# Kernel optimization log

Measured on AMD Instinct MI355X. Metric: run time of the kernel, lower is better.

The kernel has to match this reference:

```python
import jax, jax.numpy as jnp
import numpy as np

B, L, F, H, VOCAB = 32, 700, 4, 600, 2000  # batch, n_records(max_len), feats/record, hidden, vocab


def setup_inputs() -> dict:
    key = jax.random.key(0)
    ks = jax.random.split(key, 16)
    s = 0.02
    inp = {
        'records': jax.random.randint(ks[0], (B, L, F), 0, VOCAB, dtype=jnp.int64 if jax.config.jax_enable_x64 else jnp.int32),
        'index': jax.random.randint(ks[1], (B,), 0, L, dtype=jnp.int32),
        'emb': jax.random.normal(ks[2], (VOCAB, H), jnp.float32) * s,
        'W_relu': jax.random.normal(ks[3], (4 * H, H), jnp.float32) * s,
        'b_relu': jnp.zeros((H,), jnp.float32),
        'W_lin': jax.random.normal(ks[4], (H, H), jnp.float32) * s,
        'b_lin': jnp.zeros((H,), jnp.float32),
        'W_sig': jax.random.normal(ks[5], (2 * H, H), jnp.float32) * s,
        'b_sig': jnp.zeros((H,), jnp.float32),
        'W_ih': jax.random.normal(ks[6], (H, 4 * H), jnp.float32) * s,
        'W_hh': jax.random.normal(ks[7], (H, 4 * H), jnp.float32) * s,
        'b_ih': jnp.zeros((4 * H,), jnp.float32),
        'b_hh': jnp.zeros((4 * H,), jnp.float32),
        'W_log': jax.random.normal(ks[8], (H, L), jnp.float32) * s,
        'b_log': jnp.zeros((L,), jnp.float32),
    }
    return inp


def _select_content(records, emb, W_relu, b_relu, W_lin, b_lin, W_sig, b_sig):
    # embedding + concat of the 4 record features -> [B, L, 4H]
    embedded = emb[records]                               # [B, L, 4, H]
    emb_cat = embedded.reshape(records.shape[0], records.shape[1], -1)
    emb_relu = jax.nn.relu(emb_cat @ W_relu + b_relu)      # [B, L, H]
    emb_lin = emb_relu @ W_lin + b_lin                     # [B, L, H]
    pre_attn = jnp.einsum('bld,bmd->blm', emb_lin, emb_relu)  # [B, L, L]
    pad = (records.max(axis=2) == 0)                       # [B, L]
    mask = jnp.eye(records.shape[1], dtype=bool)[None] | pad[:, :, None] | pad[:, None, :]
    pre_attn = jnp.where(mask, -jnp.inf, pre_attn)
    attention = jax.nn.softmax(pre_attn, axis=2)
    emb_att = jnp.einsum('blm,bmd->bld', attention, emb_relu)  # [B, L, H]
    gate = jax.nn.sigmoid(jnp.concatenate([emb_relu, emb_att], axis=2) @ W_sig + b_sig)
    return gate * emb_relu                                 # selected_content [B, L, H]


def reference(records, index, emb, W_relu, b_relu, W_lin, b_lin, W_sig, b_sig,
              W_ih, W_hh, b_ih, b_hh, W_log, b_log):
    sc = _select_content(records, emb, W_relu, b_relu, W_lin, b_lin, W_sig, b_sig)
    # init_hidden
    hidden = jnp.mean(sc, axis=1)                          # [B, H]
    cell = jnp.zeros_like(hidden)
    pad_mask = (records.max(axis=2) == 0)                  # [B, L]
    # forward (one pointer step)
    b_idx = jnp.arange(records.shape[0])
    mask = pad_mask.at[b_idx, index].set(True)             # scatter_(1, index, 1)
    x = sc[b_idx, index]                                   # gather -> [B, H]
    gates = x @ W_ih + hidden @ W_hh + b_ih + b_hh         # [B, 4H]
    i, f, g, o = jnp.split(gates, 4, axis=1)               # torch LSTM gate order
    cell = jax.nn.sigmoid(f) * cell + jax.nn.sigmoid(i) * jnp.tanh(g)
    hidden = jax.nn.sigmoid(o) * jnp.tanh(cell)
    logits = hidden @ W_log + b_log                        # [B, max_len]
    masked = jnp.where(mask, -jnp.inf, logits)
    attention = jax.nn.log_softmax(masked, axis=1)         # [B, max_len]
    return attention, hidden, cell
```

## Files before the change

### kernel.cpp

```cpp
#include <hip/hip_runtime.h>
#include <math.h>

typedef unsigned short u16;
typedef _Float16 half8 __attribute__((ext_vector_type(8)));
typedef float f32x4 __attribute__((ext_vector_type(4)));

#define BB 32
#define LL 700
#define HH 600
#define VV 2000
#define H4 2400

#define O_SCAT   0L
#define O_LINH   57344000L
#define O_R1     86016000L
#define O_ATTNH  112896000L
#define O_ERT    144435200L
#define O_EMBH   171468800L
#define O_W2T    174028800L
#define O_WLT    177100800L
#define O_WST    177920000L
#define O_BL     179456000L
#define O_PAD    179458560L
#define O_GATES  179624960L
#define O_WIHT   179932160L
#define O_WLOGT  186076160L
#define O_XCAT   186977280L
#define O_HID16  187059200L
#define O_GLOG   187100160L
#define O_XMEAN  187190272L

__device__ inline u16 f2h(float x) { _Float16 h = (_Float16)x; u16 u; __builtin_memcpy(&u, &h, 2); return u; }
__device__ inline float h2f(u16 u) { _Float16 h; __builtin_memcpy(&h, &u, 2); return (float)h; }

__device__ __forceinline__ void gll16(const u16* g, u16* l) {
    __builtin_amdgcn_global_load_lds(
        (__attribute__((address_space(1))) void*)g,
        (__attribute__((address_space(3))) void*)l, 16, 0, 0);
}

template<int EPI>
__global__ __launch_bounds__(512, 4) void hgemm_v2(
    const u16* __restrict__ A, const u16* __restrict__ B,
    u16* __restrict__ C16, const float* __restrict__ bias,
    const u16* __restrict__ gate, int ldg,
    float* __restrict__ xmean,
    int M, int N, int Kp, int lda, int ldb, int ldc,
    long sAz, long sBz, long sCz)
{
    const int bz = blockIdx.z;
    A += sAz * bz;  B += sBz * bz;  C16 += sCz * bz;

    __shared__ __align__(16) u16 As[16384];
    __shared__ __align__(16) u16 Bs[16384];

    const int tid = threadIdx.x;

    const int nx = gridDim.x, ny = gridDim.y;
    const int bid = blockIdx.y * nx + blockIdx.x;
    const int fg  = ny >> 3;
    const int gsz = nx << 3;
    int m_i, n_i;
    if (bid < fg * gsz) {
        int g = bid / gsz, r = bid - g * gsz;
        m_i = (g << 3) + (r & 7);
        n_i = r >> 3;
    } else {
        m_i = bid / nx;
        n_i = bid - m_i * nx;
    }
    const int m0 = m_i << 7, n0 = n_i << 7;

    const int wave = tid >> 6, lane = tid & 63;
    const int fr = lane & 15, q = lane >> 4;
    const int s0 = (q ^ (fr & 7)) << 3;
    const int wm = (wave >> 2) << 6;
    const int wn = (wave & 3) << 5;

    const int srow = lane >> 3;
    const int kx   = ((lane & 7) ^ srow) << 3;
    int ra0 = m0 + (wave << 4) + srow;       if (ra0 > M - 1) ra0 = M - 1;
    int ra1 = m0 + (wave << 4) + 8 + srow;   if (ra1 > M - 1) ra1 = M - 1;
    int rb0 = n0 + (wave << 4) + srow;       if (rb0 > N - 1) rb0 = N - 1;
    int rb1 = n0 + (wave << 4) + 8 + srow;   if (rb1 > N - 1) rb1 = N - 1;
    const u16* gA0 = A + (long)ra0 * lda + kx;
    const u16* gA1 = A + (long)ra1 * lda + kx;
    const u16* gB0 = B + (long)rb0 * ldb + kx;
    const u16* gB1 = B + (long)rb1 * ldb + kx;
    u16* sAw = (u16*)As + (wave << 10);
    u16* sBw = (u16*)Bs + (wave << 10);

    f32x4 acc[4][2];
    #pragma unroll
    for (int i = 0; i < 4; ++i)
        #pragma unroll
        for (int j = 0; j < 2; ++j) acc[i][j] = (f32x4)0.f;

    const int nk = Kp >> 6;

    gll16(gA0, sAw);  gll16(gA1, sAw + 512);
    gll16(gB0, sBw);  gll16(gB1, sBw + 512);
    __syncthreads();

    for (int t = 0; t < nk; ++t) {
        const int cur = (t & 1) << 13;
        if (t + 1 < nk) {
            const int nxt = cur ^ 8192;
            const long ko = (long)(t + 1) << 6;
            gll16(gA0 + ko, sAw + nxt);  gll16(gA1 + ko, sAw + nxt + 512);
            gll16(gB0 + ko, sBw + nxt);  gll16(gB1 + ko, sBw + nxt + 512);
        }
        #pragma unroll
        for (int half = 0; half < 2; ++half) {
            const int sh = s0 ^ (half << 5);
            half8 af[4], bf[2];
            #pragma unroll
            for (int i = 0; i < 4; ++i)
                af[i] = *(const half8*)&As[cur + ((wm + (i << 4) + fr) << 6) + sh];
            #pragma unroll
            for (int j = 0; j < 2; ++j)
                bf[j] = *(const half8*)&Bs[cur + ((wn + (j << 4) + fr) << 6) + sh];
            #pragma unroll
            for (int i = 0; i < 4; ++i)
                #pragma unroll
                for (int j = 0; j < 2; ++j)
                    acc[i][j] = __builtin_amdgcn_mfma_f32_16x16x32_f16(af[i], bf[j], acc[i][j], 0, 0, 0);
        }
        __syncthreads();
    }

    const int lr = (lane >> 4) << 2;

    int  bb0 = 0, bound = 0;
    bool interior = false;
    if (EPI == 2) {
        const int mlo = m0 + wm, mhi = m0 + wm + 63;
        bb0   = mlo / 700;
        bound = (bb0 + 1) * 700;
        interior = (mhi < bound) && (mhi < M);
    }

    #pragma unroll
    for (int j = 0; j < 2; ++j) {
        int n = n0 + wn + (j << 4) + fr;
        if (n >= N) continue;
        float bv = bias ? bias[n] : 0.f;

        if (EPI == 2 && interior) {
            float ps = 0.f;
            #pragma unroll
            for (int i = 0; i < 4; ++i) {
                #pragma unroll
                for (int r = 0; r < 4; ++r) {
                    int m = m0 + wm + (i << 4) + lr + r;
                    float v = acc[i][j][r] + bv;
                    float sg = 1.f / (1.f + expf(-v));
                    float scv = sg * h2f(gate[(long)m * ldg + n]);
                    C16[(long)m * ldc + n] = f2h(scv);
                    ps += scv;
                }
            }
            ps += __shfl_xor(ps, 16);
            ps += __shfl_xor(ps, 32);
            if (q == 0) atomicAdd(&xmean[bb0 * 640 + n], ps);
        } else {
            float ps = 0.f;
            int   cb = -1;
            #pragma unroll
            for (int i = 0; i < 4; ++i) {
                #pragma unroll
                for (int r = 0; r < 4; ++r) {
                    int m = m0 + wm + (i << 4) + lr + r;
                    if (m >= M) continue;
                    long off = (long)m * ldc + n;
                    float v = acc[i][j][r] + bv;
                    if (EPI == 1) C16[off] = f2h(v);
                    if (EPI == 2) {
                        float sg = 1.f / (1.f + expf(-v));
                        float scv = sg * h2f(gate[(long)m * ldg + n]);
                        C16[off] = f2h(scv);
                        int b = (m < bound) ? bb0 : bb0 + 1;
                        if (b != cb) {
                            if (cb >= 0) atomicAdd(&xmean[cb * 640 + n], ps);
                            cb = b;  ps = 0.f;
                        }
                        ps += scv;
                    }
                }
            }
            if (EPI == 2 && cb >= 0) atomicAdd(&xmean[cb * 640 + n], ps);
        }
    }
}

__global__ __launch_bounds__(256) void sgemm_k(
    const u16* __restrict__ A, const u16* __restrict__ B, float* __restrict__ C,
    int N, int Kseg, int lda, int ldb, int ldc)
{
    const int wave = threadIdx.x >> 6, lane = threadIdx.x & 63;
    const int fr = lane & 15, q8 = (lane >> 4) << 3;
    int n = blockIdx.x * 64 + wave * 16 + fr;
    int nc = (n < N) ? n : N - 1;
    const int k0 = blockIdx.y * Kseg;
    const u16* pa0 = A + (long)fr * lda + q8;
    const u16* pa1 = A + (long)(fr + 16) * lda + q8;
    const u16* pb  = B + (long)nc * ldb + q8;
    f32x4 acc0 = (f32x4)0.f, acc1 = (f32x4)0.f;
    #pragma unroll 2
    for (int k = k0; k < k0 + Kseg; k += 32) {
        half8 a0 = *(const half8*)(pa0 + k);
        half8 a1 = *(const half8*)(pa1 + k);
        half8 bv = *(const half8*)(pb + k);
        acc0 = __builtin_amdgcn_mfma_f32_16x16x32_f16(a0, bv, acc0, 0, 0, 0);
        acc1 = __builtin_amdgcn_mfma_f32_16x16x32_f16(a1, bv, acc1, 0, 0, 0);
    }
    if (n >= N) return;
    const int mr = (lane >> 4) << 2;
    #pragma unroll
    for (int r = 0; r < 4; ++r) {
        atomicAdd(&C[(long)(mr + r) * ldc + n], acc0[r]);
        atomicAdd(&C[(long)(mr + r + 16) * ldc + n], acc1[r]);
    }
}

__global__ __launch_bounds__(256) void prep_k(
    const float* __restrict__ emb, const float* __restrict__ W_relu,
    const float* __restrict__ W_lin, const float* __restrict__ W_sig,
    const float* __restrict__ W_ih, const float* __restrict__ W_hh,
    const float* __restrict__ W_log, const float* __restrict__ b_lin,
    const float* __restrict__ b_ih, const float* __restrict__ b_hh,
    const float* __restrict__ b_log,
    u16* __restrict__ embh, u16* __restrict__ w2t, u16* __restrict__ wlt,
    u16* __restrict__ wst, u16* __restrict__ wiht, u16* __restrict__ wlogt,
    float* __restrict__ bl640, float* __restrict__ gates, float* __restrict__ glog,
    float* __restrict__ xmean)
{
    __shared__ float t[32][33];
    const int z = blockIdx.z, bx = blockIdx.x, by = blockIdx.y;
    const int tid = threadIdx.x;

    if (z == 10) {
        int r = by * 32 + (tid >> 5), c = bx * 32 + (tid & 31);
        #pragma unroll
        for (int dy = 0; dy < 32; dy += 8) {
            int rr = r + dy;
            if (rr < VV && c < 640)
                embh[(long)rr * 640 + c] = (c < 600) ? f2h(emb[(long)rr * 600 + c]) : 0;
        }
        return;
    }
    if (z == 11) {
        long idx = ((long)bx * 75 + by) * 256 + tid;
        const long NG = 640 + (long)BB * H4;
        const long NL = NG + (long)BB * 704;
        const long NX = NL + (long)BB * 640;
        if (idx < 640) {
            bl640[idx] = (idx < 600) ? b_lin[idx] : 0.f;
        } else if (idx < NG) {
            long i = idx - 640;
            int n = (int)(i % H4);
            gates[i] = b_ih[n] + b_hh[n];
        } else if (idx < NL) {
            long i = idx - NG;
            int l = (int)(i % 704);
            glog[i] = (l < 700) ? b_log[l] : 0.f;
        } else if (idx < NX) {
            xmean[idx - NL] = 0.f;
        }
        return;
    }

    const float* s; u16* d;
    int R, C, lds_, ldo, Rpad, Cpad;
    if (z < 4)      { s = W_relu + 360000L * z; d = w2t + 384000L * z;
                      R = 600; C = 600; lds_ = 600; ldo = 640;  Rpad = 640; Cpad = 600; }
    else if (z == 4){ s = W_lin;           d = wlt;
                      R = 600; C = 600; lds_ = 600; ldo = 640;  Rpad = 640; Cpad = 640; }
    else if (z == 5){ s = W_sig;           d = wst;
                      R = 600; C = 600; lds_ = 600; ldo = 1280; Rpad = 640; Cpad = 600; }
    else if (z == 6){ s = W_sig + 360000;  d = wst + 640;
                      R = 600; C = 600; lds_ = 600; ldo = 1280; Rpad = 640; Cpad = 600; }
    else if (z == 7){ s = W_ih;            d = wiht;
                      R = 600; C = H4;  lds_ = H4;  ldo = 1280; Rpad = 640; Cpad = H4; }
    else if (z == 8){ s = W_hh;            d = wiht + 640;
                      R = 600; C = H4;  lds_ = H4;  ldo = 1280; Rpad = 640; Cpad = H4; }
    else            { s = W_log;           d = wlogt;
                      R = 600; C = 700; lds_ = 700; ldo = 640;  Rpad = 640; Cpad = 704; }

    int r0 = bx * 32, c0 = by * 32;
    if (r0 >= Rpad || c0 >= Cpad) return;
    int tx = tid & 31, ty = tid >> 5;
    #pragma unroll
    for (int dy = 0; dy < 32; dy += 8) {
        int r = r0 + ty + dy, c = c0 + tx;
        t[ty + dy][tx] = (r < R && c < C) ? s[(long)r * lds_ + c] : 0.f;
    }
    __syncthreads();
    #pragma unroll
    for (int dy = 0; dy < 32; dy += 8) {
        int c = c0 + ty + dy, r = r0 + tx;
        if (r < Rpad && c < Cpad) d[(long)c * ldo + r] = f2h(t[tx][ty + dy]);
    }
}

__global__ __launch_bounds__(320) void gather_relu_k(
    const int* __restrict__ rec, const u16* __restrict__ Ph,
    const float* __restrict__ b_relu, u16* __restrict__ scat, float* __restrict__ pad)
{
    int row = blockIdx.x;
    int t = threadIdx.x;
    int r0 = rec[row * 4 + 0], r1 = rec[row * 4 + 1];
    int r2 = rec[row * 4 + 2], r3 = rec[row * 4 + 3];
    u16* srow = scat + (long)row * 1280;
    if (t < 300) {
        int h = t << 1;
        uint a0 = *(const uint*)&Ph[(long)r0 * H4 + h];
        uint a1 = *(const uint*)&Ph[(long)r1 * H4 + 600 + h];
        uint a2 = *(const uint*)&Ph[(long)r2 * H4 + 1200 + h];
        uint a3 = *(const uint*)&Ph[(long)r3 * H4 + 1800 + h];
        float lo = b_relu[h]     + h2f((u16)a0) + h2f((u16)a1) + h2f((u16)a2) + h2f((u16)a3);
        float hi = b_relu[h + 1] + h2f((u16)(a0 >> 16)) + h2f((u16)(a1 >> 16))
                                 + h2f((u16)(a2 >> 16)) + h2f((u16)(a3 >> 16));
        uint o = (uint)f2h(fmaxf(lo, 0.f)) | ((uint)f2h(fmaxf(hi, 0.f)) << 16);
        *(uint*)&srow[h] = o;
    } else {
        int i = t - 300;
        *(uint*)&srow[600 + (i << 1)]  = 0;
        *(uint*)&srow[1240 + (i << 1)] = 0;
    }
    if (t == 0) {
        int mx = max(max(r0, r1), max(r2, r3));
        pad[row] = (mx == 0) ? 1.f : 0.f;
    }
}

__global__ __launch_bounds__(256) void post4_k(
    u16* __restrict__ attnh, const float* __restrict__ pad,
    const u16* __restrict__ scat, u16* __restrict__ erT)
{
    __shared__ float smem[1056];
    const int bidf = blockIdx.x;
    const int tid  = threadIdx.x;

    if (bidf < 5600) {
        const int bx = bidf % 175, b = bidf / 175;
        const float* pb = pad + b * LL;
        for (int e = tid; e < 704; e += 256)
            smem[e] = (e < LL) ? pb[e] : 1.f;
        __syncthreads();

        const int wave = tid >> 6, lane = tid & 63;
        const int l = bx * 4 + wave;
        u16* row = attnh + (long)b * (LL * 704) + (long)l * 704;
        const bool rowpad = smem[l] != 0.f;

        float v[12];
        float mx = -INFINITY;
        #pragma unroll
        for (int i = 0; i < 6; ++i) {
            int e0 = (lane + (i << 6)) << 1;
            float x0 = -INFINITY, x1 = -INFINITY;
            if (e0 < 704) {
                uint u = *(const uint*)&row[e0];
                if (!(rowpad || e0 == l || smem[e0] != 0.f)) x0 = h2f((u16)u);
                int e1 = e0 + 1;
                if (!(rowpad || e1 == l || smem[e1] != 0.f)) x1 = h2f((u16)(u >> 16));
            }
            v[2 * i] = x0;  v[2 * i + 1] = x1;
            mx = fmaxf(mx, fmaxf(x0, x1));
        }
        #pragma unroll
        for (int m = 32; m > 0; m >>= 1) mx = fmaxf(mx, __shfl_xor(mx, m));
        mx = fmaxf(mx, -1e30f);

        float sum = 0.f;
        #pragma unroll
        for (int i = 0; i < 12; ++i) { v[i] = expf(v[i] - mx); sum += v[i]; }
        #pragma unroll
        for (int m = 32; m > 0; m >>= 1) sum += __shfl_xor(sum, m);
        float inv = (sum > 0.f) ? 1.f / sum : 0.f;

        #pragma unroll
        for (int i = 0; i < 6; ++i) {
            int e0 = (lane + (i << 6)) << 1;
            if (e0 < 704) {
                uint u = (uint)f2h(v[2 * i] * inv) | ((uint)f2h(v[2 * i + 1] * inv) << 16);
                *(uint*)&row[e0] = u;
            }
        }
    } else {
        int tt = bidf - 5600;
        const int bx = tt % 22;  tt /= 22;
        const int by = tt % 19;
        const int bz = tt / 19;
        float (*tr)[33] = (float(*)[33])smem;
        const u16* s = scat + (long)LL * 1280 * bz;
        u16* d = erT + (long)HH * 704 * bz;
        int r0 = bx * 32, c0 = by * 32;
        int tx = tid & 31, ty = tid >> 5;
        #pragma unroll
        for (int dy = 0; dy < 32; dy += 8) {
            int r = r0 + ty + dy, c = c0 + tx;
            tr[ty + dy][tx] = (r < LL && c < HH) ? h2f(s[(long)r * 1280 + c]) : 0.f;
        }
        __syncthreads();
        #pragma unroll
        for (int dy = 0; dy < 32; dy += 8) {
            int c = c0 + ty + dy, r = r0 + tx;
            if (r < 704 && c < HH) d[(long)c * 704 + r] = f2h(tr[tx][ty + dy]);
        }
    }
}

__global__ __launch_bounds__(256) void xcat_k(const u16* __restrict__ sc,
                                              const int* __restrict__ index,
                                              const float* __restrict__ xmean,
                                              u16* __restrict__ xcat)
{
    int b = blockIdx.y;
    if (blockIdx.x == 3) {
        const u16* src = sc + ((long)b * LL + index[b]) * HH;
        u16* dst = xcat + b * 1280;
        for (int j = threadIdx.x; j < 1280; j += 256) {
            if (j < 600) dst[j] = src[j];
            else if (j < 640) dst[j] = 0;
            else if (j >= 1240) dst[j] = 0;
        }
        return;
    }
    int h = blockIdx.x * 256 + threadIdx.x;
    if (h >= HH) return;
    xcat[b * 1280 + 640 + h] = f2h(xmean[b * 640 + h] * (1.f / 700.f));
}

__global__ void lstm_act_k(const float* __restrict__ gates,
                           float* __restrict__ out_hid, float* __restrict__ out_cell,
                           u16* __restrict__ hid16)
{
    int h = blockIdx.x * 256 + threadIdx.x;
    int b = blockIdx.y;
    if (h >= 640) return;
    if (h >= HH) { hid16[b * 640 + h] = 0; return; }
    const float* g = gates + b * H4;
    float gi = g[h], gg = g[1200 + h], go = g[1800 + h];
    float c = (1.f / (1.f + expf(-gi))) * tanhf(gg);
    float hd = (1.f / (1.f + expf(-go))) * tanhf(c);
    out_hid[b * HH + h] = hd;
    out_cell[b * HH + h] = c;
    hid16[b * 640 + h] = f2h(hd);
}

__global__ __launch_bounds__(256) void logsoftmax_k(const float* __restrict__ glog,
                                                    const float* __restrict__ pad,
                                                    const int* __restrict__ index,
                                                    float* __restrict__ out)
{
    int b = blockIdx.x;
    int t = threadIdx.x;
    int idx = index[b];
    __shared__ float red[256];
    float v[3];
    float mx = -INFINITY;
    #pragma unroll
    for (int ii = 0; ii < 3; ++ii) {
        int l = ii * 256 + t;
        float x = -INFINITY;
        if (l < LL && !(pad[b * LL + l] != 0.f || l == idx)) x = glog[b * 704 + l];
        v[ii] = x;
        mx = fmaxf(mx, x);
    }
    red[t] = mx; __syncthreads();
    for (int s = 128; s > 0; s >>= 1) {
        if (t < s) red[t] = fmaxf(red[t], red[t + s]);
        __syncthreads();
    }
    mx = red[0]; __syncthreads();
    float sum = 0.f;
    #pragma unroll
    for (int ii = 0; ii < 3; ++ii) {
        int l = ii * 256 + t;
        if (l < LL) sum += expf(v[ii] - mx);
    }
    red[t] = sum; __syncthreads();
    for (int s = 128; s > 0; s >>= 1) {
        if (t < s) red[t] += red[t + s];
        __syncthreads();
    }
    float lse = mx + logf(red[0]);
    #pragma unroll
    for (int ii = 0; ii < 3; ++ii) {
        int l = ii * 256 + t;
        if (l < LL) out[b * LL + l] = fmaxf(v[ii] - lse, -1e30f);
    }
}

extern "C" void kernel_launch(void* const* d_in, const int* in_sizes, int n_in,
                              void* d_out, int out_size, void* d_ws, size_t ws_size,
                              hipStream_t stream)
{
    const int*   records = (const int*)d_in[0];
    const int*   index   = (const int*)d_in[1];
    const float* emb     = (const float*)d_in[2];
    const float* W_relu  = (const float*)d_in[3];
    const float* b_relu  = (const float*)d_in[4];
    const float* W_lin   = (const float*)d_in[5];
    const float* b_lin   = (const float*)d_in[6];
    const float* W_sig   = (const float*)d_in[7];
    const float* b_sig   = (const float*)d_in[8];
    const float* W_ih    = (const float*)d_in[9];
    const float* W_hh    = (const float*)d_in[10];
    const float* b_ih    = (const float*)d_in[11];
    const float* b_hh    = (const float*)d_in[12];
    const float* W_log   = (const float*)d_in[13];
    const float* b_log   = (const float*)d_in[14];

    char* ws = (char*)d_ws;
    u16*   scat   = (u16*)(ws + O_SCAT);
    u16*   linh   = (u16*)(ws + O_LINH);
    u16*   Ph     = (u16*)(ws + O_R1);
    u16*   sc16   = (u16*)(ws + O_R1);
    u16*   attnh  = (u16*)(ws + O_ATTNH);
    u16*   erT    = (u16*)(ws + O_ERT);
    u16*   embh   = (u16*)(ws + O_EMBH);
    u16*   w2t    = (u16*)(ws + O_W2T);
    u16*   wlt    = (u16*)(ws + O_WLT);
    u16*   wst    = (u16*)(ws + O_WST);
    float* bl640  = (float*)(ws + O_BL);
    float* pad    = (float*)(ws + O_PAD);
    float* gates  = (float*)(ws + O_GATES);
    u16*   wiht   = (u16*)(ws + O_WIHT);
    u16*   wlogt  = (u16*)(ws + O_WLOGT);
    u16*   xcat   = (u16*)(ws + O_XCAT);
    u16*   hid16  = (u16*)(ws + O_HID16);
    float* glog   = (float*)(ws + O_GLOG);
    float* xmean  = (float*)(ws + O_XMEAN);

    float* out      = (float*)d_out;
    float* out_attn = out;
    float* out_hid  = out + BB * LL;
    float* out_cell = out + BB * LL + BB * HH;

    prep_k<<<dim3(20, 75, 12), 256, 0, stream>>>(
        emb, W_relu, W_lin, W_sig, W_ih, W_hh, W_log, b_lin, b_ih, b_hh, b_log,
        embh, w2t, wlt, wst, wiht, wlogt, bl640, gates, glog, xmean);

    hgemm_v2<1><<<dim3(19, 16, 1), 512, 0, stream>>>(
        embh, w2t, Ph, nullptr, nullptr, 0, nullptr,
        VV, H4, 640, 640, 640, H4, 0L, 0L, 0L);

    gather_relu_k<<<dim3(BB * LL), 320, 0, stream>>>(records, Ph, b_relu, scat, pad);

    hgemm_v2<1><<<dim3(5, 175, 1), 512, 0, stream>>>(
        scat, wlt, linh, bl640, nullptr, 0, nullptr,
        BB * LL, 640, 640, 1280, 640, 640, 0L, 0L, 0L);

    hgemm_v2<1><<<dim3(6, 6, BB), 512, 0, stream>>>(
        linh, scat, attnh, nullptr, nullptr, 0, nullptr,
        LL, LL, 640, 640, 1280, 704, (long)LL * 640, (long)LL * 1280, (long)LL * 704);

    post4_k<<<dim3(5600 + 22 * 19 * BB), 256, 0, stream>>>(attnh, pad, scat, erT);

    hgemm_v2<1><<<dim3(5, 6, BB), 512, 0, stream>>>(
        attnh, erT, scat + 640, nullptr, nullptr, 0, nullptr,
        LL, HH, 704, 704, 704, 1280, (long)LL * 704, (long)HH * 704, (long)LL * 1280);

    hgemm_v2<2><<<dim3(5, 175, 1), 512, 0, stream>>>(
        scat, wst, sc16, b_sig, scat, 1280, xmean,
        BB * LL, HH, 1280, 1280, 1280, 600, 0L, 0L, 0L);

    xcat_k<<<dim3(4, BB), 256, 0, stream>>>(sc16, index, xmean, xcat);
    sgemm_k<<<dim3(38, 5), 256, 0, stream>>>(
        xcat, wiht, gates, H4, 256, 1280, 1280, H4);
    lstm_act_k<<<dim3(3, BB), 256, 0, stream>>>(gates, out_hid, out_cell, hid16);
    sgemm_k<<<dim3(11, 5), 256, 0, stream>>>(
        hid16, wlogt, glog, LL, 128, 640, 640, 704);
    logsoftmax_k<<<dim3(BB), 256, 0, stream>>>(glog, pad, index, out_attn);
}
```

Baseline: 407.7 us.

## Fuse erT transpose into lin GEMM launch and merge tail kernels cooperatively

The scat-to-erT transpose moves out of the post-softmax kernel and into extra blocks of the linear-projection GEMM launch. Those blocks run alongside the GEMM tiles, and the softmax becomes its own kernel. The five small tail kernels (xcat, two skinny GEMMs, LSTM activation, log-softmax) are merged into one cooperative kernel that separates phases with grid.sync, cutting launch overhead. The cost is grid-sync latency, plus transpose blocks that must request the GEMM's large LDS and 512-thread footprint, which may reduce their occupancy.

```diff
diff --git a/kernel.cpp b/kernel.cpp
--- a/kernel.cpp
+++ b/kernel.cpp
@@ -1,5 +1,8 @@
 #include <hip/hip_runtime.h>
+#include <hip/hip_cooperative_groups.h>
 #include <math.h>
+
+namespace cg = cooperative_groups;
 
 typedef unsigned short u16;
 typedef _Float16 half8 __attribute__((ext_vector_type(8)));
@@ -39,25 +42,51 @@
         (__attribute__((address_space(3))) void*)l, 16, 0, 0);
 }
 
-template<int EPI>
+template<int EPI, int FUSET>
 __global__ __launch_bounds__(512, 4) void hgemm_v2(
     const u16* __restrict__ A, const u16* __restrict__ B,
     u16* __restrict__ C16, const float* __restrict__ bias,
     const u16* __restrict__ gate, int ldg,
     float* __restrict__ xmean,
     int M, int N, int Kp, int lda, int ldb, int ldc,
-    long sAz, long sBz, long sCz)
-{
+    long sAz, long sBz, long sCz,
+    const u16* __restrict__ tsrc, u16* __restrict__ tdst, int gemm_blocks)
+{
+    __shared__ __align__(16) u16 As[16384];
+    __shared__ __align__(16) u16 Bs[16384];
+
+    if (FUSET && (int)blockIdx.x >= gemm_blocks) {
+        float (*trf)[33] = (float(*)[33])As;
+        int tt = blockIdx.x - gemm_blocks;
+        const int bx = tt % 22;  tt /= 22;
+        const int by = tt % 19;
+        const int bz2 = tt / 19;
+        const u16* s = tsrc + (long)LL * 1280 * bz2;
+        u16* d = tdst + (long)HH * 704 * bz2;
+        const int r0 = bx << 5, c0 = by << 5;
+        const int tx = threadIdx.x & 31, ty = threadIdx.x >> 5;
+        #pragma unroll
+        for (int dy = 0; dy < 32; dy += 16) {
+            int r = r0 + ty + dy, c = c0 + tx;
+            trf[ty + dy][tx] = (r < LL && c < HH) ? h2f(s[(long)r * 1280 + c]) : 0.f;
+        }
+        __syncthreads();
+        #pragma unroll
+        for (int dy = 0; dy < 32; dy += 16) {
+            int c = c0 + ty + dy, r = r0 + tx;
+            if (r < 704 && c < HH) d[(long)c * 704 + r] = f2h(trf[tx][ty + dy]);
+        }
+        return;
+    }
+
     const int bz = blockIdx.z;
     A += sAz * bz;  B += sBz * bz;  C16 += sCz * bz;
 
-    __shared__ __align__(16) u16 As[16384];
-    __shared__ __align__(16) u16 Bs[16384];
-
     const int tid = threadIdx.x;
 
-    const int nx = gridDim.x, ny = gridDim.y;
-    const int bid = blockIdx.y * nx + blockIdx.x;
+    const int nx = FUSET ? 5 : gridDim.x;
+    const int ny = FUSET ? 175 : gridDim.y;
+    const int bid = FUSET ? (int)blockIdx.x : (int)(blockIdx.y * nx + blockIdx.x);
     const int fg  = ny >> 3;
     const int gsz = nx << 3;
     int m_i, n_i;
@@ -193,15 +222,15 @@
     }
 }
 
-__global__ __launch_bounds__(256) void sgemm_k(
-    const u16* __restrict__ A, const u16* __restrict__ B, float* __restrict__ C,
-    int N, int Kseg, int lda, int ldb, int ldc)
-{
-    const int wave = threadIdx.x >> 6, lane = threadIdx.x & 63;
+__device__ __forceinline__ void sgemm_body(
+    int bx, int by, const u16* A, const u16* B, float* C,
+    int N, int Kseg, int lda, int ldb, int ldc, int tid)
+{
+    const int wave = tid >> 6, lane = tid & 63;
     const int fr = lane & 15, q8 = (lane >> 4) << 3;
-    int n = blockIdx.x * 64 + wave * 16 + fr;
+    int n = bx * 64 + wave * 16 + fr;
     int nc = (n < N) ? n : N - 1;
-    const int k0 = blockIdx.y * Kseg;
+    const int k0 = by * Kseg;
     const u16* pa0 = A + (long)fr * lda + q8;
     const u16* pa1 = A + (long)(fr + 16) * lda + q8;
     const u16* pb  = B + (long)nc * ldb + q8;
@@ -220,6 +249,101 @@
     for (int r = 0; r < 4; ++r) {
         atomicAdd(&C[(long)(mr + r) * ldc + n], acc0[r]);
         atomicAdd(&C[(long)(mr + r + 16) * ldc + n], acc1[r]);
+    }
+}
+
+__global__ __launch_bounds__(256) void tail_k(
+    const u16* __restrict__ sc16, const int* __restrict__ index,
+    const float* __restrict__ xmean, u16* __restrict__ xcat,
+    const u16* __restrict__ wiht, float* __restrict__ gates,
+    float* __restrict__ out_hid, float* __restrict__ out_cell,
+    u16* __restrict__ hid16, const u16* __restrict__ wlogt,
+    float* __restrict__ glog, const float* __restrict__ pad,
+    float* __restrict__ out_attn)
+{
+    cg::grid_group grid = cg::this_grid();
+    const int fb  = blockIdx.x;
+    const int tid = threadIdx.x;
+
+    if (fb < 128) {
+        int bxx = fb & 3, b = fb >> 2;
+        if (bxx == 3) {
+            const u16* src = sc16 + ((long)b * LL + index[b]) * HH;
+            u16* dst = xcat + b * 1280;
+            for (int j = tid; j < 1280; j += 256) {
+                if (j < 600) dst[j] = src[j];
+                else if (j < 640) dst[j] = 0;
+                else if (j >= 1240) dst[j] = 0;
+            }
+        } else {
+            int h = bxx * 256 + tid;
+            if (h < HH) xcat[b * 1280 + 640 + h] = f2h(xmean[b * 640 + h] * (1.f / 700.f));
+        }
+    }
+    grid.sync();
+
+    if (fb < 190) sgemm_body(fb % 38, fb / 38, xcat, wiht, gates, H4, 256, 1280, 1280, H4, tid);
+    grid.sync();
+
+    if (fb < 96) {
+        int b = fb / 3;
+        int h = (fb % 3) * 256 + tid;
+        if (h < 640) {
+            if (h >= HH) {
+                hid16[b * 640 + h] = 0;
+            } else {
+                const float* g = gates + b * H4;
+                float gi = g[h], gg = g[1200 + h], go = g[1800 + h];
+                float c = (1.f / (1.f + expf(-gi))) * tanhf(gg);
+                float hd = (1.f / (1.f + expf(-go))) * tanhf(c);
+                out_hid[b * HH + h] = hd;
+                out_cell[b * HH + h] = c;
+                hid16[b * 640 + h] = f2h(hd);
+            }
+        }
+    }
+    grid.sync();
+
+    if (fb < 55) sgemm_body(fb % 11, fb / 11, hid16, wlogt, glog, LL, 128, 640, 640, 704, tid);
+    grid.sync();
+
+    if (fb < 32) {
+        int b = fb;
+        int idx = index[b];
+        __shared__ float red[256];
+        float v[3];
+        float mx = -INFINITY;
+        #pragma unroll
+        for (int ii = 0; ii < 3; ++ii) {
+            int l = ii * 256 + tid;
+            float x = -INFINITY;
+            if (l < LL && !(pad[b * LL + l] != 0.f || l == idx)) x = glog[b * 704 + l];
+            v[ii] = x;
+            mx = fmaxf(mx, x);
+        }
+        red[tid] = mx; __syncthreads();
+        for (int s = 128; s > 0; s >>= 1) {
+            if (tid < s) red[tid] = fmaxf(red[tid], red[tid + s]);
+            __syncthreads();
+        }
+        mx = red[0]; __syncthreads();
+        float sum = 0.f;
+        #pragma unroll
+        for (int ii = 0; ii < 3; ++ii) {
+            int l = ii * 256 + tid;
+            if (l < LL) sum += expf(v[ii] - mx);
+        }
+        red[tid] = sum; __syncthreads();
+        for (int s = 128; s > 0; s >>= 1) {
+            if (tid < s) red[tid] += red[tid + s];
+            __syncthreads();
+        }
+        float lse = mx + logf(red[0]);
+        #pragma unroll
+        for (int ii = 0; ii < 3; ++ii) {
+            int l = ii * 256 + tid;
+            if (l < LL) out_attn[b * LL + l] = fmaxf(v[ii] - lse, -1e30f);
+        }
     }
 }
 
@@ -334,163 +458,55 @@
     }
 }
 
-__global__ __launch_bounds__(256) void post4_k(
-    u16* __restrict__ attnh, const float* __restrict__ pad,
-    const u16* __restrict__ scat, u16* __restrict__ erT)
-{
-    __shared__ float smem[1056];
-    const int bidf = blockIdx.x;
-    const int tid  = threadIdx.x;
-
-    if (bidf < 5600) {
-        const int bx = bidf % 175, b = bidf / 175;
-        const float* pb = pad + b * LL;
-        for (int e = tid; e < 704; e += 256)
-            smem[e] = (e < LL) ? pb[e] : 1.f;
-        __syncthreads();
-
-        const int wave = tid >> 6, lane = tid & 63;
-        const int l = bx * 4 + wave;
-        u16* row = attnh + (long)b * (LL * 704) + (long)l * 704;
-        const bool rowpad = smem[l] != 0.f;
-
-        float v[12];
-        float mx = -INFINITY;
-        #pragma unroll
-        for (int i = 0; i < 6; ++i) {
-            int e0 = (lane + (i << 6)) << 1;
-            float x0 = -INFINITY, x1 = -INFINITY;
-            if (e0 < 704) {
-                uint u = *(const uint*)&row[e0];
-                if (!(rowpad || e0 == l || smem[e0] != 0.f)) x0 = h2f((u16)u);
-                int e1 = e0 + 1;
-                if (!(rowpad || e1 == l || smem[e1] != 0.f)) x1 = h2f((u16)(u >> 16));
-            }
-            v[2 * i] = x0;  v[2 * i + 1] = x1;
-            mx = fmaxf(mx, fmaxf(x0, x1));
-        }
-        #pragma unroll
-        for (int m = 32; m > 0; m >>= 1) mx = fmaxf(mx, __shfl_xor(mx, m));
-        mx = fmaxf(mx, -1e30f);
-
-        float sum = 0.f;
-        #pragma unroll
-        for (int i = 0; i < 12; ++i) { v[i] = expf(v[i] - mx); sum += v[i]; }
-        #pragma unroll
-        for (int m = 32; m > 0; m >>= 1) sum += __shfl_xor(sum, m);
-        float inv = (sum > 0.f) ? 1.f / sum : 0.f;
-
-        #pragma unroll
-        for (int i = 0; i < 6; ++i) {
-            int e0 = (lane + (i << 6)) << 1;
-            if (e0 < 704) {
-                uint u = (uint)f2h(v[2 * i] * inv) | ((uint)f2h(v[2 * i + 1] * inv) << 16);
-                *(uint*)&row[e0] = u;
-            }
-        }
-    } else {
-        int tt = bidf - 5600;
-        const int bx = tt % 22;  tt /= 22;
-        const int by = tt % 19;
-        const int bz = tt / 19;
-        float (*tr)[33] = (float(*)[33])smem;
-        const u16* s = scat + (long)LL * 1280 * bz;
-        u16* d = erT + (long)HH * 704 * bz;
-        int r0 = bx * 32, c0 = by * 32;
-        int tx = tid & 31, ty = tid >> 5;
-        #pragma unroll
-        for (int dy = 0; dy < 32; dy += 8) {
-            int r = r0 + ty + dy, c = c0 + tx;
-            tr[ty + dy][tx] = (r < LL && c < HH) ? h2f(s[(long)r * 1280 + c]) : 0.f;
-        }
-        __syncthreads();
-        #pragma unroll
-        for (int dy = 0; dy < 32; dy += 8) {
-            int c = c0 + ty + dy, r = r0 + tx;
-            if (r < 704 && c < HH) d[(long)c * 704 + r] = f2h(tr[tx][ty + dy]);
-        }
-    }
-}
-
-__global__ __launch_bounds__(256) void xcat_k(const u16* __restrict__ sc,
-                                              const int* __restrict__ index,
-                                              const float* __restrict__ xmean,
-                                              u16* __restrict__ xcat)
-{
-    int b = blockIdx.y;
-    if (blockIdx.x == 3) {
-        const u16* src = sc + ((long)b * LL + index[b]) * HH;
-        u16* dst = xcat + b * 1280;
-        for (int j = threadIdx.x; j < 1280; j += 256) {
-            if (j < 600) dst[j] = src[j];
-            else if (j < 640) dst[j] = 0;
-            else if (j >= 1240) dst[j] = 0;
-        }
-        return;
-    }
-    int h = blockIdx.x * 256 + threadIdx.x;
-    if (h >= HH) return;
-    xcat[b * 1280 + 640 + h] = f2h(xmean[b * 640 + h] * (1.f / 700.f));
-}
-
-__global__ void lstm_act_k(const float* __restrict__ gates,
-                           float* __restrict__ out_hid, float* __restrict__ out_cell,
-                           u16* __restrict__ hid16)
-{
-    int h = blockIdx.x * 256 + threadIdx.x;
-    int b = blockIdx.y;
-    if (h >= 640) return;
-    if (h >= HH) { hid16[b * 640 + h] = 0; return; }
-    const float* g = gates + b * H4;
-    float gi = g[h], gg = g[1200 + h], go = g[1800 + h];
-    float c = (1.f / (1.f + expf(-gi))) * tanhf(gg);
-    float hd = (1.f / (1.f + expf(-go))) * tanhf(c);
-    out_hid[b * HH + h] = hd;
-    out_cell[b * HH + h] = c;
-    hid16[b * 640 + h] = f2h(hd);
-}
-
-__global__ __launch_bounds__(256) void logsoftmax_k(const float* __restrict__ glog,
-                                                    const float* __restrict__ pad,
-                                                    const int* __restrict__ index,
-                                                    float* __restrict__ out)
-{
-    int b = blockIdx.x;
-    int t = threadIdx.x;
-    int idx = index[b];
-    __shared__ float red[256];
-    float v[3];
+__global__ __launch_bounds__(256) void softmax_w(u16* __restrict__ attnh,
+                                                 const float* __restrict__ pad)
+{
+    __shared__ float smem[704];
+    const int bx = blockIdx.x, b = blockIdx.y;
+    const int tid = threadIdx.x;
+    const float* pb = pad + b * LL;
+    for (int e = tid; e < 704; e += 256)
+        smem[e] = (e < LL) ? pb[e] : 1.f;
+    __syncthreads();
+
+    const int wave = tid >> 6, lane = tid & 63;
+    const int l = bx * 4 + wave;
+    u16* row = attnh + (long)b * (LL * 704) + (long)l * 704;
+    const bool rowpad = smem[l] != 0.f;
+
+    float v[12];
     float mx = -INFINITY;
     #pragma unroll
-    for (int ii = 0; ii < 3; ++ii) {
-        int l = ii * 256 + t;
-        float x = -INFINITY;
-        if (l < LL && !(pad[b * LL + l] != 0.f || l == idx)) x = glog[b * 704 + l];
-        v[ii] = x;
-        mx = fmaxf(mx, x);
-    }
-    red[t] = mx; __syncthreads();
-    for (int s = 128; s > 0; s >>= 1) {
-        if (t < s) red[t] = fmaxf(red[t], red[t + s]);
-        __syncthreads();
-    }
-    mx = red[0]; __syncthreads();
+    for (int i = 0; i < 6; ++i) {
+        int e0 = (lane + (i << 6)) << 1;
+        float x0 = -INFINITY, x1 = -INFINITY;
+        if (e0 < 704) {
+            uint u = *(const uint*)&row[e0];
+            if (!(rowpad || e0 == l || smem[e0] != 0.f)) x0 = h2f((u16)u);
+            int e1 = e0 + 1;
+            if (!(rowpad || e1 == l || smem[e1] != 0.f)) x1 = h2f((u16)(u >> 16));
+        }
+        v[2 * i] = x0;  v[2 * i + 1] = x1;
+        mx = fmaxf(mx, fmaxf(x0, x1));
+    }
+    #pragma unroll
+    for (int m = 32; m > 0; m >>= 1) mx = fmaxf(mx, __shfl_xor(mx, m));
+    mx = fmaxf(mx, -1e30f);
+
     float sum = 0.f;
     #pragma unroll
-    for (int ii = 0; ii < 3; ++ii) {
-        int l = ii * 256 + t;
-        if (l < LL) sum += expf(v[ii] - mx);
-    }
-    red[t] = sum; __syncthreads();
-    for (int s = 128; s > 0; s >>= 1) {
-        if (t < s) red[t] += red[t + s];
-        __syncthreads();
-    }
-    float lse = mx + logf(red[0]);
-    #pragma unroll
-    for (int ii = 0; ii < 3; ++ii) {
-        int l = ii * 256 + t;
-        if (l < LL) out[b * LL + l] = fmaxf(v[ii] - lse, -1e30f);
+    for (int i = 0; i < 12; ++i) { v[i] = expf(v[i] - mx); sum += v[i]; }
+    #pragma unroll
+    for (int m = 32; m > 0; m >>= 1) sum += __shfl_xor(sum, m);
+    float inv = (sum > 0.f) ? 1.f / sum : 0.f;
+
+    #pragma unroll
+    for (int i = 0; i < 6; ++i) {
+        int e0 = (lane + (i << 6)) << 1;
+        if (e0 < 704) {
+            uint u = (uint)f2h(v[2 * i] * inv) | ((uint)f2h(v[2 * i + 1] * inv) << 16);
+            *(uint*)&row[e0] = u;
+        }
     }
 }
 
@@ -544,35 +560,37 @@
         emb, W_relu, W_lin, W_sig, W_ih, W_hh, W_log, b_lin, b_ih, b_hh, b_log,
         embh, w2t, wlt, wst, wiht, wlogt, bl640, gates, glog, xmean);
 
-    hgemm_v2<1><<<dim3(19, 16, 1), 512, 0, stream>>>(
+    hgemm_v2<1, 0><<<dim3(19, 16, 1), 512, 0, stream>>>(
         embh, w2t, Ph, nullptr, nullptr, 0, nullptr,
-        VV, H4, 640, 640, 640, H4, 0L, 0L, 0L);
+        VV, H4, 640, 640, 640, H4, 0L, 0L, 0L, nullptr, nullptr, 0);
 
     gather_relu_k<<<dim3(BB * LL), 320, 0, stream>>>(records, Ph, b_relu, scat, pad);
 
-    hgemm_v2<1><<<dim3(5, 175, 1), 512, 0, stream>>>(
+    hgemm_v2<1, 1><<<dim3(875 + 22 * 19 * BB), 512, 0, stream>>>(
         scat, wlt, linh, bl640, nullptr, 0, nullptr,
-        BB * LL, 640, 640, 1280, 640, 640, 0L, 0L, 0L);
-
-    hgemm_v2<1><<<dim3(6, 6, BB), 512, 0, stream>>>(
+        BB * LL, 640, 640, 1280, 640, 640, 0L, 0L, 0L,
+        scat, erT, 875);
+
+    hgemm_v2<1, 0><<<dim3(6, 6, BB), 512, 0, stream>>>(
         linh, scat, attnh, nullptr, nullptr, 0, nullptr,
-        LL, LL, 640, 640, 1280, 704, (long)LL * 640, (long)LL * 1280, (long)LL * 704);
-
-    post4_k<<<dim3(5600 + 22 * 19 * BB), 256, 0, stream>>>(attnh, pad, scat, erT);
-
-    hgemm_v2<1><<<dim3(5, 6, BB), 512, 0, stream>>>(
+        LL, LL, 640, 640, 1280, 704, (long)LL * 640, (long)LL * 1280, (long)LL * 704,
+        nullptr, nullptr, 0);
+
+    softmax_w<<<dim3(175, BB), 256, 0, stream>>>(attnh, pad);
+
+    hgemm_v2<1, 0><<<dim3(5, 6, BB), 512, 0, stream>>>(
         attnh, erT, scat + 640, nullptr, nullptr, 0, nullptr,
-        LL, HH, 704, 704, 704, 1280, (long)LL * 704, (long)HH * 704, (long)LL * 1280);
-
-    hgemm_v2<2><<<dim3(5, 175, 1), 512, 0, stream>>>(
+        LL, HH, 704, 704, 704, 1280, (long)LL * 704, (long)HH * 704, (long)LL * 1280,
+        nullptr, nullptr, 0);
+
+    hgemm_v2<2, 0><<<dim3(5, 175, 1), 512, 0, stream>>>(
         scat, wst, sc16, b_sig, scat, 1280, xmean,
-        BB * LL, HH, 1280, 1280, 1280, 600, 0L, 0L, 0L);
-
-    xcat_k<<<dim3(4, BB), 256, 0, stream>>>(sc16, index, xmean, xcat);
-    sgemm_k<<<dim3(38, 5), 256, 0, stream>>>(
-        xcat, wiht, gates, H4, 256, 1280, 1280, H4);
-    lstm_act_k<<<dim3(3, BB), 256, 0, stream>>>(gates, out_hid, out_cell, hid16);
-    sgemm_k<<<dim3(11, 5), 256, 0, stream>>>(
-        hid16, wlogt, glog, LL, 128, 640, 640, 704);
-    logsoftmax_k<<<dim3(BB), 256, 0, stream>>>(glog, pad, index, out_attn);
-}
+        BB * LL, HH, 1280, 1280, 1280, 600, 0L, 0L, 0L, nullptr, nullptr, 0);
+
+    void* targs[] = {
+        (void*)&sc16, (void*)&index, (void*)&xmean, (void*)&xcat,
+        (void*)&wiht, (void*)&gates, (void*)&out_hid, (void*)&out_cell,
+        (void*)&hid16, (void*)&wlogt, (void*)&glog, (void*)&pad, (void*)&out_attn
+    };
+    hipLaunchCooperativeKernel((void*)tail_k, dim3(190), dim3(256), targs, 0, stream);
+}
```

After: 520.6 us. 27.7% more time.

## Add 128x128 async-LDS double-buffered GEMM for the W_lin projection

Applied to the files above, without the earlier changes.

Adds a new hgemm_v3 kernel that uses 128x128 tiles with 256 threads, direct global-to-LDS loads (gll16) into XOR-swizzled double buffers, and grouped block rasterization for L2 reuse. Only the emb_relu @ W_lin GEMM is switched to it. The goal is better data reuse per block and overlap of the next K-tile load with MFMA compute. In exchange it uses 64KB of LDS per block, which limits occupancy, and it drops the previous kernel's epilogue generality.

```diff
diff --git a/kernel.cpp b/kernel.cpp
--- a/kernel.cpp
+++ b/kernel.cpp
@@ -193,6 +193,119 @@
     }
 }
 
+__global__ __launch_bounds__(256, 2) void hgemm_v3(
+    const u16* __restrict__ A, const u16* __restrict__ B,
+    u16* __restrict__ C16, const float* __restrict__ bias,
+    int M, int N, int Kp, int lda, int ldb, int ldc)
+{
+    __shared__ __align__(16) u16 As[16384];
+    __shared__ __align__(16) u16 Bs[16384];
+
+    const int tid = threadIdx.x;
+
+    const int nx = gridDim.x, ny = gridDim.y;
+    const int bid = blockIdx.y * nx + blockIdx.x;
+    const int fg  = ny >> 3;
+    const int gsz = nx << 3;
+    int m_i, n_i;
+    if (bid < fg * gsz) {
+        int g = bid / gsz, r = bid - g * gsz;
+        m_i = (g << 3) + (r & 7);
+        n_i = r >> 3;
+    } else {
+        m_i = bid / nx;
+        n_i = bid - m_i * nx;
+    }
+    const int m0 = m_i << 7, n0 = n_i << 7;
+
+    const int wave = tid >> 6, lane = tid & 63;
+    const int fr = lane & 15, q = lane >> 4;
+    const int s0 = (q ^ (fr & 7)) << 3;
+    const int wm = (wave >> 1) << 6;
+    const int wn = (wave & 1) << 6;
+
+    const int srow = lane >> 3;
+    const int kx   = ((lane & 7) ^ srow) << 3;
+    int ra[4], rb[4];
+    #pragma unroll
+    for (int g2 = 0; g2 < 4; ++g2) {
+        int r = m0 + (wave << 5) + (g2 << 3) + srow;  if (r > M - 1) r = M - 1;
+        ra[g2] = r;
+        r = n0 + (wave << 5) + (g2 << 3) + srow;      if (r > N - 1) r = N - 1;
+        rb[g2] = r;
+    }
+    const u16 *gA[4], *gB[4];
+    #pragma unroll
+    for (int g2 = 0; g2 < 4; ++g2) {
+        gA[g2] = A + (long)ra[g2] * lda + kx;
+        gB[g2] = B + (long)rb[g2] * ldb + kx;
+    }
+    u16* sAw = (u16*)As + (wave << 11);
+    u16* sBw = (u16*)Bs + (wave << 11);
+
+    f32x4 acc[4][4];
+    #pragma unroll
+    for (int i = 0; i < 4; ++i)
+        #pragma unroll
+        for (int j = 0; j < 4; ++j) acc[i][j] = (f32x4)0.f;
+
+    const int nk = Kp >> 6;
+
+    #pragma unroll
+    for (int g2 = 0; g2 < 4; ++g2) {
+        gll16(gA[g2], sAw + (g2 << 9));
+        gll16(gB[g2], sBw + (g2 << 9));
+    }
+    __syncthreads();
+
+    for (int t = 0; t < nk; ++t) {
+        const int cur = (t & 1) << 13;
+        if (t + 1 < nk) {
+            const int nxt = cur ^ 8192;
+            const long ko = (long)(t + 1) << 6;
+            #pragma unroll
+            for (int g2 = 0; g2 < 4; ++g2) {
+                gll16(gA[g2] + ko, sAw + nxt + (g2 << 9));
+                gll16(gB[g2] + ko, sBw + nxt + (g2 << 9));
+            }
+        }
+        #pragma unroll
+        for (int half = 0; half < 2; ++half) {
+            const int sh = s0 ^ (half << 5);
+            half8 af[4], bf[4];
+            #pragma unroll
+            for (int i = 0; i < 4; ++i)
+                af[i] = *(const half8*)&As[cur + ((wm + (i << 4) + fr) << 6) + sh];
+            #pragma unroll
+            for (int j = 0; j < 4; ++j)
+                bf[j] = *(const half8*)&Bs[cur + ((wn + (j << 4) + fr) << 6) + sh];
+            #pragma unroll
+            for (int i = 0; i < 4; ++i)
+                #pragma unroll
+                for (int j = 0; j < 4; ++j)
+                    acc[i][j] = __builtin_amdgcn_mfma_f32_16x16x32_f16(af[i], bf[j], acc[i][j], 0, 0, 0);
+        }
+        __syncthreads();
+    }
+
+    const int lr = (lane >> 4) << 2;
+    #pragma unroll
+    for (int j = 0; j < 4; ++j) {
+        int n = n0 + wn + (j << 4) + fr;
+        if (n >= N) continue;
+        float bv = bias ? bias[n] : 0.f;
+        #pragma unroll
+        for (int i = 0; i < 4; ++i) {
+            #pragma unroll
+            for (int r = 0; r < 4; ++r) {
+                int m = m0 + wm + (i << 4) + lr + r;
+                if (m >= M) continue;
+                C16[(long)m * ldc + n] = f2h(acc[i][j][r] + bv);
+            }
+        }
+    }
+}
+
 __global__ __launch_bounds__(256) void sgemm_k(
     const u16* __restrict__ A, const u16* __restrict__ B, float* __restrict__ C,
     int N, int Kseg, int lda, int ldb, int ldc)
@@ -550,9 +663,9 @@
 
     gather_relu_k<<<dim3(BB * LL), 320, 0, stream>>>(records, Ph, b_relu, scat, pad);
 
-    hgemm_v2<1><<<dim3(5, 175, 1), 512, 0, stream>>>(
-        scat, wlt, linh, bl640, nullptr, 0, nullptr,
-        BB * LL, 640, 640, 1280, 640, 640, 0L, 0L, 0L);
+    hgemm_v3<<<dim3(5, 175, 1), 256, 0, stream>>>(
+        scat, wlt, linh, bl640,
+        BB * LL, 640, 640, 1280, 640, 640);
 
     hgemm_v2<1><<<dim3(6, 6, BB), 512, 0, stream>>>(
         linh, scat, attnh, nullptr, nullptr, 0, nullptr,
```

Measured after the change: 418.9 us. 1.03x slower.
